# Optimization experiments

Measured on AMD Instinct MI355X. Metric: run time of the kernel, lower is better.

The kernel has to match this reference:

```python
import jax, jax.numpy as jnp
import numpy as np
import math

D_MODEL = 1024
N_HEADS = 16
D_FF = 4096
B, S = 4, 2048
EPS = 1e-5


def _layernorm(x, g, b):
    mu = jnp.mean(x, axis=-1, keepdims=True)
    var = jnp.mean(jnp.square(x - mu), axis=-1, keepdims=True)
    return (x - mu) * jax.lax.rsqrt(var + EPS) * g + b


def setup_inputs() -> dict:
    key = jax.random.key(0)
    ks = jax.random.split(key, 16)
    D, F = D_MODEL, D_FF
    s = 1.0 / math.sqrt(D)
    sf = 1.0 / math.sqrt(F)
    return {
        "x": jax.random.normal(ks[0], (B, S, D), jnp.float32),
        "mask": jnp.ones((B, 1, 1, S), jnp.int32),
        "Wq": jax.random.uniform(ks[1], (D, D), jnp.float32, -s, s),
        "bq": jnp.zeros((D,), jnp.float32),
        "Wk": jax.random.uniform(ks[2], (D, D), jnp.float32, -s, s),
        "bk": jnp.zeros((D,), jnp.float32),
        "Wv": jax.random.uniform(ks[3], (D, D), jnp.float32, -s, s),
        "bv": jnp.zeros((D,), jnp.float32),
        "Wo": jax.random.uniform(ks[4], (D, D), jnp.float32, -s, s),
        "bo": jnp.zeros((D,), jnp.float32),
        "W1": jax.random.uniform(ks[5], (D, F), jnp.float32, -s, s),
        "b1": jnp.zeros((F,), jnp.float32),
        "W2": jax.random.uniform(ks[6], (F, D), jnp.float32, -sf, sf),
        "b2": jnp.zeros((D,), jnp.float32),
        "g1": jnp.ones((D,), jnp.float32),
        "be1": jnp.zeros((D,), jnp.float32),
        "g2": jnp.ones((D,), jnp.float32),
        "be2": jnp.zeros((D,), jnp.float32),
    }


def reference(x, mask, Wq, bq, Wk, bk, Wv, bv, Wo, bo, W1, b1, W2, b2, g1, be1, g2, be2):
    Bb, Ss, D = x.shape
    H = N_HEADS
    hd = D // H
    # QKV projections -> [B, H, S, hd]
    q = (x @ Wq + bq).reshape(Bb, Ss, H, hd).transpose(0, 2, 1, 3)
    k = (x @ Wk + bk).reshape(Bb, Ss, H, hd).transpose(0, 2, 1, 3)
    v = (x @ Wv + bv).reshape(Bb, Ss, H, hd).transpose(0, 2, 1, 3)
    # explicit O(S^2) attention, as in the source
    scores = jnp.einsum("bhqd,bhkd->bhqk", q, k) / math.sqrt(hd)
    scores = jnp.where(mask == 0, jnp.float32(-1e9), scores)
    attn = jax.nn.softmax(scores, axis=-1)
    o = jnp.einsum("bhqk,bhkd->bhqd", attn, v)
    o = o.transpose(0, 2, 1, 3).reshape(Bb, Ss, D)
    attn_out = o @ Wo + bo
    # residual + LN (dropout in eval mode = identity)
    h = _layernorm(x + attn_out, g1, be1)
    ff = jax.nn.relu(h @ W1 + b1) @ W2 + b2
    return _layernorm(h + ff, g2, be2)
```

## Files before the change

### kernel.cpp

```cpp
#include <hip/hip_runtime.h>
#include <hip/hip_bf16.h>
#include <stdint.h>

typedef __bf16 bf16;
typedef __bf16 bf16x8 __attribute__((ext_vector_type(8)));
typedef __bf16 bf16x4 __attribute__((ext_vector_type(4)));
typedef float f32x4 __attribute__((ext_vector_type(4)));
typedef unsigned short u16;

__device__ __forceinline__ float b2f(bf16 v) { return (float)v; }
__device__ __forceinline__ bf16 f2b(float f) { return (bf16)f; }

#define GLD16(gp, lp)                                              \
  __builtin_amdgcn_global_load_lds(                                \
      (const __attribute__((address_space(1))) void*)(gp),         \
      (__attribute__((address_space(3))) void*)(lp), 16, 0, 0)

__device__ __forceinline__ float ldval(const void* p, size_t i, int isf32) {
  return isf32 ? ((const float*)p)[i] : b2f(((const bf16*)p)[i]);
}

__global__ void sniff_kernel(const void* x, int* flag) {
  __shared__ int smax[256];
  int tid = threadIdx.x;
  const u16* p = (const u16*)x;
  int mx = 0;
  for (int i = tid; i < 8192; i += 256) {
    int e = (p[i] >> 7) & 0xFF;
    mx = mx > e ? mx : e;
  }
  smax[tid] = mx;
  __syncthreads();
  for (int s = 128; s > 0; s >>= 1) {
    if (tid < s) smax[tid] = smax[tid] > smax[tid + s] ? smax[tid] : smax[tid + s];
    __syncthreads();
  }
  if (tid == 0) *flag = (smax[0] >= 135) ? 1 : 0;
}

__global__ void cvt_kernel(const void* __restrict__ in, bf16* __restrict__ out,
                           int n, const int* __restrict__ flag) {
  int f = *flag;
  int i = blockIdx.x * 256 + threadIdx.x;
  if (i < n) out[i] = f2b(ldval(in, i, f));
}

__global__ void transpose_k(const void* __restrict__ in, bf16* __restrict__ out,
                            int K, int N, const int* __restrict__ flag) {
  int f = *flag;
  __shared__ bf16 tile[32][33];
  int bn = blockIdx.x * 32, bk = blockIdx.y * 32;
  int tx = threadIdx.x, ty = threadIdx.y;
#pragma unroll
  for (int i = 0; i < 32; i += 8)
    tile[ty + i][tx] = f2b(ldval(in, (size_t)(bk + ty + i) * N + bn + tx, f));
  __syncthreads();
#pragma unroll
  for (int i = 0; i < 32; i += 8)
    out[(size_t)(bn + ty + i) * K + bk + tx] = tile[tx][ty + i];
}

template <int ACT, int GROUP>
__global__ __launch_bounds__(256, 3)
void gemm_bt(const bf16* __restrict__ A, const bf16* __restrict__ Bt,
             const bf16* __restrict__ bias, bf16* __restrict__ C,
             int M, int N, int K) {
  __shared__ __attribute__((aligned(16))) bf16 As[128][64];
  __shared__ __attribute__((aligned(16))) bf16 Bs[128][64];
  __shared__ __attribute__((aligned(16))) bf16 Cs[32][136];
  const int tid = threadIdx.x;
  const int wave = tid >> 6;
  const int lane = tid & 63;

  const int grid_n = N >> 7;
  const int pid = blockIdx.x;
  const int xcd = pid & 7;
  const int j = pid >> 3;
  const int per = GROUP * grid_n;
  const int chunk = j / per;
  const int r0 = j - chunk * per;
  const int mb = xcd * 8 + chunk * GROUP + (r0 & (GROUP - 1));
  const int nb = r0 / GROUP;
  const int m0 = mb * 128;
  const int n0 = nb * 128;

  const int wr = (wave >> 1) * 64;
  const int wc = (wave & 1) * 64;
  const int row_q = lane & 15;
  const int quad = lane >> 4;

  const f32x4 fz = {0.f, 0.f, 0.f, 0.f};
  f32x4 acc[4][4];
#pragma unroll
  for (int i = 0; i < 4; i++)
#pragma unroll
    for (int jj = 0; jj < 4; jj++) acc[i][jj] = fz;

  int srow[4], sck[4];
#pragma unroll
  for (int i = 0; i < 4; i++) {
    int c = i * 256 + tid;
    srow[i] = c >> 3;
    sck[i] = (c & 7) * 8;
  }

  for (int k0 = 0; k0 < K; k0 += 64) {
    __syncthreads();
#pragma unroll
    for (int i = 0; i < 4; i++) {
      GLD16(A + (size_t)(m0 + srow[i]) * K + k0 + sck[i], &As[srow[i]][sck[i]]);
      GLD16(Bt + (size_t)(n0 + srow[i]) * K + k0 + sck[i], &Bs[srow[i]][sck[i]]);
    }
    __syncthreads();
#pragma unroll
    for (int ks = 0; ks < 2; ks++) {
      bf16x8 af[4], bfr[4];
      int cf = ks * 4 + quad;
#pragma unroll
      for (int mi = 0; mi < 4; mi++)
        af[mi] = *(const bf16x8*)&As[wr + mi * 16 + row_q][cf * 8];
#pragma unroll
      for (int ni = 0; ni < 4; ni++)
        bfr[ni] = *(const bf16x8*)&Bs[wc + ni * 16 + row_q][cf * 8];
#pragma unroll
      for (int mi = 0; mi < 4; mi++)
#pragma unroll
        for (int ni = 0; ni < 4; ni++)
          acc[mi][ni] = __builtin_amdgcn_mfma_f32_16x16x32_bf16(
              af[mi], bfr[ni], acc[mi][ni], 0, 0, 0);
    }
  }

#pragma unroll
  for (int p = 0; p < 4; p++) {
    __syncthreads();
    if ((wave >> 1) == (p >> 1)) {
#pragma unroll
      for (int ni = 0; ni < 4; ni++) {
        int col = wc + ni * 16 + row_q;
        float bval = b2f(bias[n0 + col]);
#pragma unroll
        for (int mi2 = 0; mi2 < 2; mi2++) {
          int mi = (p & 1) * 2 + mi2;
#pragma unroll
          for (int reg = 0; reg < 4; reg++) {
            int lr = mi2 * 16 + quad * 4 + reg;
            float v = acc[mi][ni][reg] + bval;
            if (ACT == 1) v = v > 0.f ? v : 0.f;
            Cs[lr][col] = f2b(v);
          }
        }
      }
    }
    __syncthreads();
#pragma unroll
    for (int i = 0; i < 2; i++) {
      int u = i * 256 + tid;
      int row = u >> 4;
      int cu = u & 15;
      uint4 v = *(const uint4*)&Cs[row][cu * 8];
      *(uint4*)&C[(size_t)(m0 + p * 32 + row) * N + n0 + cu * 8] = v;
    }
  }
}

template <int GROUP>
__global__ __launch_bounds__(256, 3)
void gemm_btv(const bf16* __restrict__ A, const bf16* __restrict__ Bt,
              const bf16* __restrict__ bias, bf16* __restrict__ Vg,
              int M, int N, int K) {
  __shared__ __attribute__((aligned(16))) bf16 As[128][64];
  __shared__ __attribute__((aligned(16))) bf16 Bs[128][64];
  __shared__ __attribute__((aligned(16))) bf16 Ct[32][136];
  const int tid = threadIdx.x;
  const int wave = tid >> 6;
  const int lane = tid & 63;

  const int grid_n = N >> 7;
  const int pid = blockIdx.x;
  const int xcd = pid & 7;
  const int j = pid >> 3;
  const int per = GROUP * grid_n;
  const int chunk = j / per;
  const int r0 = j - chunk * per;
  const int mb = xcd * 8 + chunk * GROUP + (r0 & (GROUP - 1));
  const int nb = r0 / GROUP;
  const int m0 = mb * 128;
  const int n0 = nb * 128;

  const int wr = (wave >> 1) * 64;
  const int wc = (wave & 1) * 64;
  const int row_q = lane & 15;
  const int quad = lane >> 4;

  const f32x4 fz = {0.f, 0.f, 0.f, 0.f};
  f32x4 acc[4][4];
#pragma unroll
  for (int i = 0; i < 4; i++)
#pragma unroll
    for (int jj = 0; jj < 4; jj++) acc[i][jj] = fz;

  int srow[4], sck[4];
#pragma unroll
  for (int i = 0; i < 4; i++) {
    int c = i * 256 + tid;
    srow[i] = c >> 3;
    sck[i] = (c & 7) * 8;
  }

  for (int k0 = 0; k0 < K; k0 += 64) {
    __syncthreads();
#pragma unroll
    for (int i = 0; i < 4; i++) {
      GLD16(A + (size_t)(m0 + srow[i]) * K + k0 + sck[i], &As[srow[i]][sck[i]]);
      GLD16(Bt + (size_t)(n0 + srow[i]) * K + k0 + sck[i], &Bs[srow[i]][sck[i]]);
    }
    __syncthreads();
#pragma unroll
    for (int ks = 0; ks < 2; ks++) {
      bf16x8 af[4], bfr[4];
      int cf = ks * 4 + quad;
#pragma unroll
      for (int mi = 0; mi < 4; mi++)
        af[mi] = *(const bf16x8*)&As[wr + mi * 16 + row_q][cf * 8];
#pragma unroll
      for (int ni = 0; ni < 4; ni++)
        bfr[ni] = *(const bf16x8*)&Bs[wc + ni * 16 + row_q][cf * 8];
#pragma unroll
      for (int mi = 0; mi < 4; mi++)
#pragma unroll
        for (int ni = 0; ni < 4; ni++)
          acc[mi][ni] = __builtin_amdgcn_mfma_f32_16x16x32_bf16(
              af[mi], bfr[ni], acc[mi][ni], 0, 0, 0);
    }
  }

  const int b = m0 >> 11;
  const int s0 = m0 & 2047;
#pragma unroll
  for (int p = 0; p < 4; p++) {
    __syncthreads();
    if ((wave & 1) == (p >> 1)) {
#pragma unroll
      for (int ni2 = 0; ni2 < 2; ni2++) {
        int ni = (p & 1) * 2 + ni2;
        int cl = ni2 * 16 + row_q;
        float bval = b2f(bias[n0 + p * 32 + cl]);
#pragma unroll
        for (int mi = 0; mi < 4; mi++)
#pragma unroll
          for (int reg = 0; reg < 4; reg++) {
            int row = wr + mi * 16 + quad * 4 + reg;
            Ct[cl][row] = f2b(acc[mi][ni][reg] + bval);
          }
      }
    }
    __syncthreads();
#pragma unroll
    for (int i = 0; i < 2; i++) {
      int u = i * 256 + tid;
      int cl = u >> 4;
      int rc = u & 15;
      uint4 v = *(const uint4*)&Ct[cl][rc * 8];
      *(uint4*)&Vg[(size_t)(b * 1024 + n0 + p * 32 + cl) * 2048 + s0 + rc * 8] = v;
    }
  }
}

#define BC 128
__global__ __launch_bounds__(256, 3)
void attn_kernel(const bf16* __restrict__ QKb, const bf16* __restrict__ Vg,
                 const int* __restrict__ mask, bf16* __restrict__ O) {
  __shared__ __attribute__((aligned(16))) bf16 Ks[BC][72];
  __shared__ __attribute__((aligned(16))) bf16 Vt[64][136];
  __shared__ __attribute__((aligned(16))) bf16 Ps[4][16][136];
  const int tid = threadIdx.x;
  const int wave = tid >> 6, lane = tid & 63;
  const int pid = blockIdx.x;
  const int xcd = pid & 7;
  const int jj = pid >> 3;
  const int bh = xcd * 8 + (jj >> 5);
  const int b = bh >> 4, h = bh & 15;
  const int q0 = (jj & 31) * 64;
  const int row_q = lane & 15, quad = lane >> 4;

  bf16x8 qf[2];
  {
    int qrow = q0 + wave * 16 + row_q;
    const bf16* qp = QKb + (size_t)(b * 2048 + qrow) * 2048 + h * 64 + quad * 8;
    qf[0] = *(const bf16x8*)qp;
    qf[1] = *(const bf16x8*)(qp + 32);
#pragma unroll
    for (int ks = 0; ks < 2; ks++)
#pragma unroll
      for (int e = 0; e < 8; e++) qf[ks][e] = f2b(b2f(qf[ks][e]) * 0.125f);
  }
  float m_i = -1e30f, l_i = 0.f;
  const f32x4 fz = {0.f, 0.f, 0.f, 0.f};
  f32x4 o_acc[4];
#pragma unroll
  for (int d = 0; d < 4; d++) o_acc[d] = fz;

  int ki[4], kdc[4], vd[4], vkc[4];
#pragma unroll
  for (int j = 0; j < 4; j++) {
    int c = j * 256 + tid;
    ki[j] = c >> 3;  kdc[j] = (c & 7) * 8;
    vd[j] = c >> 4;  vkc[j] = (c & 15) * 8;
  }
  const bf16* Kbase = QKb + (size_t)b * 2048 * 2048 + 1024 + h * 64;
  const bf16* Vbase = Vg + (size_t)(b * 1024 + h * 64) * 2048;
  const int* mrow = mask + b * 2048;

  for (int kb = 0; kb < 2048 / BC; kb++) {
    __syncthreads();
    {
      uint4 kv0[4], vv0[4];
#pragma unroll
      for (int j = 0; j < 4; j++) {
        kv0[j] = *(const uint4*)(Kbase + (size_t)(kb * BC + ki[j]) * 2048 + kdc[j]);
        vv0[j] = *(const uint4*)(Vbase + (size_t)vd[j] * 2048 + kb * BC + vkc[j]);
      }
#pragma unroll
      for (int j = 0; j < 4; j++) {
        *(uint4*)&Ks[ki[j]][kdc[j]] = kv0[j];
        *(uint4*)&Vt[vd[j]][vkc[j]] = vv0[j];
      }
    }
    __syncthreads();
    int2 mm = *(const int2*)&mrow[kb * BC + lane * 2];
    bool allok = (__ballot((mm.x != 0) & (mm.y != 0)) == ~0ull);

    f32x4 sacc[8];
#pragma unroll
    for (int nt = 0; nt < 8; nt++) sacc[nt] = fz;
#pragma unroll
    for (int ks = 0; ks < 2; ks++) {
#pragma unroll
      for (int nt = 0; nt < 8; nt++) {
        bf16x8 kf = *(const bf16x8*)&Ks[nt * 16 + row_q][ks * 32 + quad * 8];
        sacc[nt] = __builtin_amdgcn_mfma_f32_16x16x32_bf16(kf, qf[ks], sacc[nt], 0, 0, 0);
      }
    }
    float s[8][4];
#pragma unroll
    for (int nt = 0; nt < 8; nt++)
#pragma unroll
      for (int r = 0; r < 4; r++) s[nt][r] = sacc[nt][r];
    if (!allok) {
#pragma unroll
      for (int nt = 0; nt < 8; nt++) {
        int4 m4 = *(const int4*)&mrow[kb * BC + nt * 16 + quad * 4];
#pragma unroll
        for (int r = 0; r < 4; r++)
          if (((const int*)&m4)[r] == 0) s[nt][r] = -1e9f;
      }
    }
    float mq[8];
#pragma unroll
    for (int nt = 0; nt < 8; nt++)
      mq[nt] = fmaxf(fmaxf(s[nt][0], s[nt][1]), fmaxf(s[nt][2], s[nt][3]));
    float mx = fmaxf(fmaxf(fmaxf(mq[0], mq[1]), fmaxf(mq[2], mq[3])),
                     fmaxf(fmaxf(mq[4], mq[5]), fmaxf(mq[6], mq[7])));
    mx = fmaxf(mx, __shfl_xor(mx, 16));
    mx = fmaxf(mx, __shfl_xor(mx, 32));
    float mnew = fmaxf(m_i, mx);
    float alpha = __expf(m_i - mnew);
    m_i = mnew;
    float rs = 0.f;
#pragma unroll
    for (int nt = 0; nt < 8; nt++) {
      float p0 = __expf(s[nt][0] - mnew);
      float p1 = __expf(s[nt][1] - mnew);
      float p2 = __expf(s[nt][2] - mnew);
      float p3 = __expf(s[nt][3] - mnew);
      rs += (p0 + p1) + (p2 + p3);
      bf16x4 pv = {f2b(p0), f2b(p1), f2b(p2), f2b(p3)};
      *(bf16x4*)&Ps[wave][row_q][nt * 16 + quad * 4] = pv;
    }
    rs += __shfl_xor(rs, 16);
    rs += __shfl_xor(rs, 32);
    l_i = l_i * alpha + rs;
    float al[4];
#pragma unroll
    for (int r = 0; r < 4; r++) al[r] = __shfl(alpha, quad * 4 + r);
#pragma unroll
    for (int d = 0; d < 4; d++)
#pragma unroll
      for (int r = 0; r < 4; r++) o_acc[d][r] *= al[r];
#pragma unroll
    for (int kst = 0; kst < 4; kst++) {
      bf16x8 pf = *(const bf16x8*)&Ps[wave][row_q][kst * 32 + quad * 8];
#pragma unroll
      for (int d = 0; d < 4; d++) {
        bf16x8 vf = *(const bf16x8*)&Vt[d * 16 + row_q][kst * 32 + quad * 8];
        o_acc[d] = __builtin_amdgcn_mfma_f32_16x16x32_bf16(pf, vf, o_acc[d], 0, 0, 0);
      }
    }
  }
  float lv[4];
#pragma unroll
  for (int r = 0; r < 4; r++) lv[r] = __shfl(l_i, quad * 4 + r);
#pragma unroll
  for (int d = 0; d < 4; d++) {
#pragma unroll
    for (int r = 0; r < 4; r++) {
      int row = q0 + wave * 16 + quad * 4 + r;
      float v = o_acc[d][r] / fmaxf(lv[r], 1e-20f);
      O[(size_t)(b * 2048 + row) * 1024 + h * 64 + d * 16 + row_q] = f2b(v);
    }
  }
}

__global__ __launch_bounds__(256)
void ln_kernel(const bf16* __restrict__ a, const bf16* __restrict__ res,
               const bf16* __restrict__ g, const bf16* __restrict__ be,
               bf16* __restrict__ out) {
  const int row = blockIdx.x;
  const int tid = threadIdx.x;
  __shared__ float red[8];
  float xs[4], sum = 0.f, sq = 0.f;
  const size_t base = (size_t)row * 1024;
#pragma unroll
  for (int i = 0; i < 4; i++) {
    int idx = i * 256 + tid;
    float x = b2f(a[base + idx]) + b2f(res[base + idx]);
    xs[i] = x; sum += x; sq += x * x;
  }
#pragma unroll
  for (int off = 1; off < 64; off <<= 1) {
    sum += __shfl_xor(sum, off);
    sq += __shfl_xor(sq, off);
  }
  int wave = tid >> 6, lane = tid & 63;
  if (lane == 0) { red[wave] = sum; red[4 + wave] = sq; }
  __syncthreads();
  sum = red[0] + red[1] + red[2] + red[3];
  sq = red[4] + red[5] + red[6] + red[7];
  float mu = sum * (1.f / 1024.f);
  float var = sq * (1.f / 1024.f) - mu * mu;
  float rstd = rsqrtf(fmaxf(var, 0.f) + 1e-5f);
#pragma unroll
  for (int i = 0; i < 4; i++) {
    int idx = i * 256 + tid;
    float y = (xs[i] - mu) * rstd * b2f(g[idx]) + b2f(be[idx]);
    out[base + idx] = f2b(y);
  }
}

__global__ __launch_bounds__(256)
void ln_out_kernel(const bf16* __restrict__ a, const bf16* __restrict__ res,
                   const bf16* __restrict__ g, const bf16* __restrict__ be,
                   void* __restrict__ out, const int* __restrict__ flag) {
  const int f = *flag;
  const int row = blockIdx.x;
  const int tid = threadIdx.x;
  __shared__ float red[8];
  float xs[4], sum = 0.f, sq = 0.f;
  const size_t base = (size_t)row * 1024;
#pragma unroll
  for (int i = 0; i < 4; i++) {
    int idx = i * 256 + tid;
    float x = b2f(a[base + idx]) + b2f(res[base + idx]);
    xs[i] = x; sum += x; sq += x * x;
  }
#pragma unroll
  for (int off = 1; off < 64; off <<= 1) {
    sum += __shfl_xor(sum, off);
    sq += __shfl_xor(sq, off);
  }
  int wave = tid >> 6, lane = tid & 63;
  if (lane == 0) { red[wave] = sum; red[4 + wave] = sq; }
  __syncthreads();
  sum = red[0] + red[1] + red[2] + red[3];
  sq = red[4] + red[5] + red[6] + red[7];
  float mu = sum * (1.f / 1024.f);
  float var = sq * (1.f / 1024.f) - mu * mu;
  float rstd = rsqrtf(fmaxf(var, 0.f) + 1e-5f);
#pragma unroll
  for (int i = 0; i < 4; i++) {
    int idx = i * 256 + tid;
    float y = (xs[i] - mu) * rstd * b2f(g[idx]) + b2f(be[idx]);
    if (f) ((float*)out)[base + idx] = y;
    else   ((bf16*)out)[base + idx] = f2b(y);
  }
}

extern "C" void kernel_launch(void* const* d_in, const int* in_sizes, int n_in,
                              void* d_out, int out_size, void* d_ws, size_t ws_size,
                              hipStream_t stream) {
  (void)in_sizes; (void)n_in; (void)out_size; (void)ws_size;
  const void* x   = d_in[0];
  const int* mask = (const int*)d_in[1];
  const void* Wq  = d_in[2];
  const void* bq  = d_in[3];
  const void* Wk  = d_in[4];
  const void* bk  = d_in[5];
  const void* Wv  = d_in[6];
  const void* bv  = d_in[7];
  const void* Wo  = d_in[8];
  const void* bo  = d_in[9];
  const void* W1  = d_in[10];
  const void* b1  = d_in[11];
  const void* W2  = d_in[12];
  const void* b2  = d_in[13];
  const void* g1  = d_in[14];
  const void* be1 = d_in[15];
  const void* g2  = d_in[16];
  const void* be2 = d_in[17];

  char* ws = (char*)d_ws;
  bf16* xb    = (bf16*)(ws + 0);
  bf16* WqkvT = (bf16*)(ws + 16777216);
  bf16* WoT   = (bf16*)(ws + 23068672);
  bf16* W1T   = (bf16*)(ws + 25165824);
  bf16* W2T   = (bf16*)(ws + 33554432);
  bf16* sv    = (bf16*)(ws + 41943040);
  bf16* bqkvB = sv;
  bf16* boB   = sv + 3072;
  bf16* b1B   = sv + 4096;
  bf16* b2B   = sv + 8192;
  bf16* g1B   = sv + 9216;
  bf16* be1B  = sv + 10240;
  bf16* g2B   = sv + 11264;
  bf16* be2B  = sv + 12288;
  int*  flag  = (int*)(ws + 41943040 + 26624);
  bf16* QKb   = (bf16*)(ws + 41975808);
  bf16* Vg    = (bf16*)(ws + 75530240);
  bf16* Obuf  = (bf16*)(ws + 92307456);
  bf16* hbuf  = (bf16*)(ws + 109084672);
  bf16* attnp = (bf16*)(ws + 41975808);
  bf16* ff1   = (bf16*)(ws + 41975808);
  bf16* ff2o  = (bf16*)(ws + 0);

  sniff_kernel<<<1, 256, 0, stream>>>(x, flag);

  cvt_kernel<<<32768, 256, 0, stream>>>(x, xb, 8388608, flag);
  cvt_kernel<<<4, 256, 0, stream>>>(bq, bqkvB, 1024, flag);
  cvt_kernel<<<4, 256, 0, stream>>>(bk, bqkvB + 1024, 1024, flag);
  cvt_kernel<<<4, 256, 0, stream>>>(bv, bqkvB + 2048, 1024, flag);
  cvt_kernel<<<4, 256, 0, stream>>>(bo, boB, 1024, flag);
  cvt_kernel<<<16, 256, 0, stream>>>(b1, b1B, 4096, flag);
  cvt_kernel<<<4, 256, 0, stream>>>(b2, b2B, 1024, flag);
  cvt_kernel<<<4, 256, 0, stream>>>(g1, g1B, 1024, flag);
  cvt_kernel<<<4, 256, 0, stream>>>(be1, be1B, 1024, flag);
  cvt_kernel<<<4, 256, 0, stream>>>(g2, g2B, 1024, flag);
  cvt_kernel<<<4, 256, 0, stream>>>(be2, be2B, 1024, flag);

  dim3 tb(32, 8);
  transpose_k<<<dim3(32, 32), tb, 0, stream>>>(Wq, WqkvT, 1024, 1024, flag);
  transpose_k<<<dim3(32, 32), tb, 0, stream>>>(Wk, WqkvT + 1024 * 1024, 1024, 1024, flag);
  transpose_k<<<dim3(32, 32), tb, 0, stream>>>(Wv, WqkvT + 2048 * 1024, 1024, 1024, flag);
  transpose_k<<<dim3(32, 32), tb, 0, stream>>>(Wo, WoT, 1024, 1024, flag);
  transpose_k<<<dim3(128, 32), tb, 0, stream>>>(W1, W1T, 1024, 4096, flag);
  transpose_k<<<dim3(32, 128), tb, 0, stream>>>(W2, W2T, 4096, 1024, flag);

  gemm_bt<0, 8><<<1024, 256, 0, stream>>>(xb, WqkvT, bqkvB, QKb, 8192, 2048, 1024);
  gemm_btv<8><<<512, 256, 0, stream>>>(xb, WqkvT + 2048 * 1024, bqkvB + 2048, Vg,
                                       8192, 1024, 1024);
  attn_kernel<<<2048, 256, 0, stream>>>(QKb, Vg, mask, Obuf);
  gemm_bt<0, 8><<<512, 256, 0, stream>>>(Obuf, WoT, boB, attnp, 8192, 1024, 1024);
  ln_kernel<<<8192, 256, 0, stream>>>(xb, attnp, g1B, be1B, hbuf);
  gemm_bt<1, 8><<<2048, 256, 0, stream>>>(hbuf, W1T, b1B, ff1, 8192, 4096, 1024);
  gemm_bt<0, 4><<<512, 256, 0, stream>>>(ff1, W2T, b2B, ff2o, 8192, 1024, 4096);
  ln_out_kernel<<<8192, 256, 0, stream>>>(hbuf, ff2o, g2B, be2B, d_out, flag);
}
```

Baseline: 661.8 us.

## Use direct global-to-LDS loads with XOR swizzle, lazy rescale, batch prep kernels

```diff
diff --git a/kernel.cpp b/kernel.cpp
--- a/kernel.cpp
+++ b/kernel.cpp
@@ -45,11 +45,55 @@
   if (i < n) out[i] = f2b(ldval(in, i, f));
 }
 
-__global__ void transpose_k(const void* __restrict__ in, bf16* __restrict__ out,
-                            int K, int N, const int* __restrict__ flag) {
+__global__ void cvt_biases_kernel(const void* bq, const void* bk, const void* bv,
+                                  const void* bo, const void* b1, const void* b2,
+                                  const void* g1, const void* be1, const void* g2,
+                                  const void* be2, bf16* __restrict__ sv,
+                                  const int* __restrict__ flag) {
+  int f = *flag;
+  int i = blockIdx.x * 256 + threadIdx.x;
+  if (i >= 13312) return;
+  int seg = i >> 10;
+  int off = i & 1023;
+  const void* src;
+  switch (seg) {
+    case 0: src = bq; break;
+    case 1: src = bk; break;
+    case 2: src = bv; break;
+    case 3: src = bo; break;
+    case 4: case 5: case 6: case 7: src = b1; off = i - 4096; break;
+    case 8: src = b2; break;
+    case 9: src = g1; break;
+    case 10: src = be1; break;
+    case 11: src = g2; break;
+    default: src = be2; break;
+  }
+  sv[i] = f2b(ldval(src, off, f));
+}
+
+__global__ void transpose_all(const void* Wq, const void* Wk, const void* Wv,
+                              const void* Wo, const void* W1, const void* W2,
+                              bf16* WqkvT, bf16* WoT, bf16* W1T, bf16* W2T,
+                              const int* __restrict__ flag) {
   int f = *flag;
   __shared__ bf16 tile[32][33];
-  int bn = blockIdx.x * 32, bk = blockIdx.y * 32;
+  int blk = blockIdx.x;
+  const void* in; bf16* out; int K, N, bx, by;
+  if (blk < 4096) {
+    int w = blk >> 10, t = blk & 1023;
+    bx = t & 31; by = t >> 5; K = 1024; N = 1024;
+    if (w == 0)      { in = Wq; out = WqkvT; }
+    else if (w == 1) { in = Wk; out = WqkvT + 1024 * 1024; }
+    else if (w == 2) { in = Wv; out = WqkvT + 2048 * 1024; }
+    else             { in = Wo; out = WoT; }
+  } else if (blk < 8192) {
+    int t = blk - 4096; bx = t & 127; by = t >> 7; K = 1024; N = 4096;
+    in = W1; out = W1T;
+  } else {
+    int t = blk - 8192; bx = t & 31; by = t >> 5; K = 4096; N = 1024;
+    in = W2; out = W2T;
+  }
+  int bn = bx * 32, bk = by * 32;
   int tx = threadIdx.x, ty = threadIdx.y;
 #pragma unroll
   for (int i = 0; i < 32; i += 8)
@@ -271,8 +315,8 @@
 __global__ __launch_bounds__(256, 3)
 void attn_kernel(const bf16* __restrict__ QKb, const bf16* __restrict__ Vg,
                  const int* __restrict__ mask, bf16* __restrict__ O) {
-  __shared__ __attribute__((aligned(16))) bf16 Ks[BC][72];
-  __shared__ __attribute__((aligned(16))) bf16 Vt[64][136];
+  __shared__ __attribute__((aligned(16))) bf16 Ks[BC][64];
+  __shared__ __attribute__((aligned(16))) bf16 Vt[64][128];
   __shared__ __attribute__((aligned(16))) bf16 Ps[4][16][136];
   const int tid = threadIdx.x;
   const int wave = tid >> 6, lane = tid & 63;
@@ -301,32 +345,28 @@
 #pragma unroll
   for (int d = 0; d < 4; d++) o_acc[d] = fz;
 
-  int ki[4], kdc[4], vd[4], vkc[4];
+  int ki[4], kdc[4], ksc[4], vd[4], vkc[4], vsc[4];
 #pragma unroll
   for (int j = 0; j < 4; j++) {
     int c = j * 256 + tid;
-    ki[j] = c >> 3;  kdc[j] = (c & 7) * 8;
-    vd[j] = c >> 4;  vkc[j] = (c & 15) * 8;
+    ki[j] = c >> 3;  kdc[j] = c & 7;   ksc[j] = (c & 7) ^ (ki[j] & 7);
+    vd[j] = c >> 4;  vkc[j] = c & 15;  vsc[j] = (c & 15) ^ (vd[j] & 7);
   }
   const bf16* Kbase = QKb + (size_t)b * 2048 * 2048 + 1024 + h * 64;
   const bf16* Vbase = Vg + (size_t)(b * 1024 + h * 64) * 2048;
   const int* mrow = mask + b * 2048;
+  const int swz = row_q & 7;
 
   for (int kb = 0; kb < 2048 / BC; kb++) {
     __syncthreads();
-    {
-      uint4 kv0[4], vv0[4];
-#pragma unroll
-      for (int j = 0; j < 4; j++) {
-        kv0[j] = *(const uint4*)(Kbase + (size_t)(kb * BC + ki[j]) * 2048 + kdc[j]);
-        vv0[j] = *(const uint4*)(Vbase + (size_t)vd[j] * 2048 + kb * BC + vkc[j]);
-      }
-#pragma unroll
-      for (int j = 0; j < 4; j++) {
-        *(uint4*)&Ks[ki[j]][kdc[j]] = kv0[j];
-        *(uint4*)&Vt[vd[j]][vkc[j]] = vv0[j];
-      }
-    }
+#pragma unroll
+    for (int j = 0; j < 4; j++)
+      GLD16(Kbase + (size_t)(kb * BC + ki[j]) * 2048 + ksc[j] * 8,
+            &Ks[ki[j]][kdc[j] * 8]);
+#pragma unroll
+    for (int j = 0; j < 4; j++)
+      GLD16(Vbase + (size_t)vd[j] * 2048 + kb * BC + vsc[j] * 8,
+            &Vt[vd[j]][vkc[j] * 8]);
     __syncthreads();
     int2 mm = *(const int2*)&mrow[kb * BC + lane * 2];
     bool allok = (__ballot((mm.x != 0) & (mm.y != 0)) == ~0ull);
@@ -336,64 +376,65 @@
     for (int nt = 0; nt < 8; nt++) sacc[nt] = fz;
 #pragma unroll
     for (int ks = 0; ks < 2; ks++) {
+      int kcf = ((ks * 4 + quad) ^ swz) * 8;
 #pragma unroll
       for (int nt = 0; nt < 8; nt++) {
-        bf16x8 kf = *(const bf16x8*)&Ks[nt * 16 + row_q][ks * 32 + quad * 8];
+        bf16x8 kf = *(const bf16x8*)&Ks[nt * 16 + row_q][kcf];
         sacc[nt] = __builtin_amdgcn_mfma_f32_16x16x32_bf16(kf, qf[ks], sacc[nt], 0, 0, 0);
       }
     }
-    float s[8][4];
-#pragma unroll
-    for (int nt = 0; nt < 8; nt++)
-#pragma unroll
-      for (int r = 0; r < 4; r++) s[nt][r] = sacc[nt][r];
     if (!allok) {
 #pragma unroll
       for (int nt = 0; nt < 8; nt++) {
         int4 m4 = *(const int4*)&mrow[kb * BC + nt * 16 + quad * 4];
 #pragma unroll
         for (int r = 0; r < 4; r++)
-          if (((const int*)&m4)[r] == 0) s[nt][r] = -1e9f;
+          if (((const int*)&m4)[r] == 0) sacc[nt][r] = -1e9f;
       }
     }
     float mq[8];
 #pragma unroll
     for (int nt = 0; nt < 8; nt++)
-      mq[nt] = fmaxf(fmaxf(s[nt][0], s[nt][1]), fmaxf(s[nt][2], s[nt][3]));
+      mq[nt] = fmaxf(fmaxf(sacc[nt][0], sacc[nt][1]),
+                     fmaxf(sacc[nt][2], sacc[nt][3]));
     float mx = fmaxf(fmaxf(fmaxf(mq[0], mq[1]), fmaxf(mq[2], mq[3])),
                      fmaxf(fmaxf(mq[4], mq[5]), fmaxf(mq[6], mq[7])));
     mx = fmaxf(mx, __shfl_xor(mx, 16));
     mx = fmaxf(mx, __shfl_xor(mx, 32));
-    float mnew = fmaxf(m_i, mx);
-    float alpha = __expf(m_i - mnew);
-    m_i = mnew;
+    if (!__all(mx - m_i <= 5.0f)) {
+      float mnew = fmaxf(m_i, mx);
+      float alpha = __expf(m_i - mnew);
+      m_i = mnew;
+      l_i *= alpha;
+      float al[4];
+#pragma unroll
+      for (int r = 0; r < 4; r++) al[r] = __shfl(alpha, quad * 4 + r);
+#pragma unroll
+      for (int d = 0; d < 4; d++)
+#pragma unroll
+        for (int r = 0; r < 4; r++) o_acc[d][r] *= al[r];
+    }
     float rs = 0.f;
 #pragma unroll
     for (int nt = 0; nt < 8; nt++) {
-      float p0 = __expf(s[nt][0] - mnew);
-      float p1 = __expf(s[nt][1] - mnew);
-      float p2 = __expf(s[nt][2] - mnew);
-      float p3 = __expf(s[nt][3] - mnew);
+      float p0 = __expf(sacc[nt][0] - m_i);
+      float p1 = __expf(sacc[nt][1] - m_i);
+      float p2 = __expf(sacc[nt][2] - m_i);
+      float p3 = __expf(sacc[nt][3] - m_i);
       rs += (p0 + p1) + (p2 + p3);
       bf16x4 pv = {f2b(p0), f2b(p1), f2b(p2), f2b(p3)};
       *(bf16x4*)&Ps[wave][row_q][nt * 16 + quad * 4] = pv;
     }
     rs += __shfl_xor(rs, 16);
     rs += __shfl_xor(rs, 32);
-    l_i = l_i * alpha + rs;
-    float al[4];
-#pragma unroll
-    for (int r = 0; r < 4; r++) al[r] = __shfl(alpha, quad * 4 + r);
-#pragma unroll
-    for (int d = 0; d < 4; d++)
-#pragma unroll
-      for (int r = 0; r < 4; r++) o_acc[d][r] *= al[r];
+    l_i += rs;
 #pragma unroll
     for (int kst = 0; kst < 4; kst++) {
       bf16x8 pf = *(const bf16x8*)&Ps[wave][row_q][kst * 32 + quad * 8];
+      int vcf = ((kst * 4 + quad) ^ swz) * 8;
 #pragma unroll
       for (int d = 0; d < 4; d++) {
-        bf16x8 vf = *(const bf16x8*)&Vt[d * 16 + row_q][kst * 32 + quad * 8];
+        bf16x8 vf = *(const bf16x8*)&Vt[d * 16 + row_q][vcf];
         o_acc[d] = __builtin_amdgcn_mfma_f32_16x16x32_bf16(pf, vf, o_acc[d], 0, 0, 0);
       }
     }
@@ -536,24 +577,12 @@
   sniff_kernel<<<1, 256, 0, stream>>>(x, flag);
 
   cvt_kernel<<<32768, 256, 0, stream>>>(x, xb, 8388608, flag);
-  cvt_kernel<<<4, 256, 0, stream>>>(bq, bqkvB, 1024, flag);
-  cvt_kernel<<<4, 256, 0, stream>>>(bk, bqkvB + 1024, 1024, flag);
-  cvt_kernel<<<4, 256, 0, stream>>>(bv, bqkvB + 2048, 1024, flag);
-  cvt_kernel<<<4, 256, 0, stream>>>(bo, boB, 1024, flag);
-  cvt_kernel<<<16, 256, 0, stream>>>(b1, b1B, 4096, flag);
-  cvt_kernel<<<4, 256, 0, stream>>>(b2, b2B, 1024, flag);
-  cvt_kernel<<<4, 256, 0, stream>>>(g1, g1B, 1024, flag);
-  cvt_kernel<<<4, 256, 0, stream>>>(be1, be1B, 1024, flag);
-  cvt_kernel<<<4, 256, 0, stream>>>(g2, g2B, 1024, flag);
-  cvt_kernel<<<4, 256, 0, stream>>>(be2, be2B, 1024, flag);
+  cvt_biases_kernel<<<52, 256, 0, stream>>>(bq, bk, bv, bo, b1, b2, g1, be1,
+                                            g2, be2, sv, flag);
 
   dim3 tb(32, 8);
-  transpose_k<<<dim3(32, 32), tb, 0, stream>>>(Wq, WqkvT, 1024, 1024, flag);
-  transpose_k<<<dim3(32, 32), tb, 0, stream>>>(Wk, WqkvT + 1024 * 1024, 1024, 1024, flag);
-  transpose_k<<<dim3(32, 32), tb, 0, stream>>>(Wv, WqkvT + 2048 * 1024, 1024, 1024, flag);
-  transpose_k<<<dim3(32, 32), tb, 0, stream>>>(Wo, WoT, 1024, 1024, flag);
-  transpose_k<<<dim3(128, 32), tb, 0, stream>>>(W1, W1T, 1024, 4096, flag);
-  transpose_k<<<dim3(32, 128), tb, 0, stream>>>(W2, W2T, 4096, 1024, flag);
+  transpose_all<<<12288, tb, 0, stream>>>(Wq, Wk, Wv, Wo, W1, W2,
+                                          WqkvT, WoT, W1T, W2T, flag);
 
   gemm_bt<0, 8><<<1024, 256, 0, stream>>>(xb, WqkvT, bqkvB, QKb, 8192, 2048, 1024);
   gemm_btv<8><<<512, 256, 0, stream>>>(xb, WqkvT + 2048 * 1024, bqkvB + 2048, Vg,
```

Result: faster. 615.7 us (-7.0%).
